# Kernel optimization log

Hardware: AMD Instinct MI355X
Metric: run time of the kernel (lower is better)

## Reference

```python
import jax, jax.numpy as jnp
import numpy as np

WIN = 8
SHIFT = 4
HEADS = 8


def _rel_pos_index(ws):
    # static numpy computation matching the torch buffer
    coords = np.stack(np.meshgrid(np.arange(ws), np.arange(ws), indexing='ij'))  # (2, ws, ws)
    cf = coords.reshape(2, -1)                      # (2, N)
    rel = cf[:, :, None] - cf[:, None, :]           # (2, N, N)
    rel = rel.transpose(1, 2, 0).copy()             # (N, N, 2)
    rel[:, :, 0] += ws - 1
    rel[:, :, 1] += ws - 1
    rel[:, :, 0] *= 2 * ws - 1
    return rel.sum(-1)                              # (N, N) int


def _attn_mask(H, W, ws, ss):
    # static shift mask, numpy (shapes are static under jit)
    img = np.zeros((H, W))
    cnt = 0
    sl = (slice(0, -ws), slice(-ws, -ss), slice(-ss, None))
    for h in sl:
        for w in sl:
            img[h, w] = cnt
            cnt += 1
    mw = img.reshape(H // ws, ws, W // ws, ws).transpose(0, 2, 1, 3).reshape(-1, ws * ws)
    diff = mw[:, None, :] - mw[:, :, None]          # (nW, N, N), matches unsqueeze(1)-unsqueeze(2)
    return np.where(diff != 0, -100.0, 0.0).astype(np.float32)


def setup_inputs() -> dict:
    key = jax.random.key(0)
    ks = jax.random.split(key, 6)
    B, C, H, W = 4, 192, 256, 256
    return {
        'x': jax.random.normal(ks[0], (B, C, H, W), jnp.float32),
        'qkv_w': jax.random.normal(ks[1], (3 * C, C), jnp.float32) * 0.02,
        'qkv_b': jnp.zeros((3 * C,), jnp.float32),
        'proj_w': jax.random.normal(ks[2], (C, C), jnp.float32) * 0.02,
        'proj_b': jnp.zeros((C,), jnp.float32),
        'rpb_table': jax.random.normal(ks[3], ((2 * WIN - 1) ** 2, HEADS), jnp.float32) * 0.02,
    }


def reference(x, qkv_w, qkv_b, proj_w, proj_b, rpb_table):
    B, C, H, W = x.shape
    ws, ss, h = WIN, SHIFT, HEADS
    N = ws * ws
    hd = C // h
    scale = hd ** -0.5

    xh = jnp.transpose(x, (0, 2, 3, 1))                       # (B,H,W,C)
    xs = jnp.roll(xh, shift=(-ss, -ss), axis=(1, 2))          # cyclic shift
    # window partition -> (B*nW, N, C)
    xw = xs.reshape(B, H // ws, ws, W // ws, ws, C).transpose(0, 1, 3, 2, 4, 5).reshape(-1, N, C)

    qkv = xw @ qkv_w.T + qkv_b                                # (B_, N, 3C)
    qkv = qkv.reshape(-1, N, 3, h, hd).transpose(2, 0, 3, 1, 4)
    q, k, v = qkv[0], qkv[1], qkv[2]                          # (B_, h, N, hd)

    attn = (q * scale) @ jnp.swapaxes(k, -2, -1)              # (B_, h, N, N)

    rpi = _rel_pos_index(ws)
    bias = rpb_table[rpi.reshape(-1)].reshape(N, N, h).transpose(2, 0, 1)  # (h, N, N)
    attn = attn + bias[None]

    mask = jnp.asarray(_attn_mask(H, W, ws, ss))              # (nW, N, N)
    nW = mask.shape[0]
    attn = attn.reshape(B, nW, h, N, N) + mask[None, :, None]
    attn = jax.nn.softmax(attn.reshape(-1, h, N, N), axis=-1)

    out = (attn @ v).transpose(0, 2, 1, 3).reshape(-1, N, C)  # (B_, N, C)
    out = out @ proj_w.T + proj_b

    # window reverse
    out = out.reshape(B, H // ws, W // ws, ws, ws, C).transpose(0, 1, 3, 2, 4, 5).reshape(B, H, W, C)
    out = jnp.roll(out, shift=(ss, ss), axis=(1, 2))          # reverse shift
    return x + jnp.transpose(out, (0, 3, 1, 2))               # residual, (B,C,H,W)
```

## Files before the change

kernel.cpp:

```cpp
#include <hip/hip_runtime.h>


typedef short short8 __attribute__((ext_vector_type(8)));
typedef float f32x4 __attribute__((ext_vector_type(4)));
typedef unsigned short us4 __attribute__((ext_vector_type(4)));

#define XB_OFF   0
#define KQ_OFF   12288
#define VT_OFF   24576
#define PB_OFF   24576
#define RPB_OFF  38400
#define QB_OFF   40200
#define LDS_BYTES 81552

#define WBF_BYTES 294912u
#define Y_FLOATS_PER_WIN 12288
#define Y_BYTES (4096ull * 49152ull)
#define WS_NEED (WBF_BYTES + Y_BYTES)

__device__ __forceinline__ unsigned short f2bfu(float f) {
  union { float f; unsigned u; } v; v.f = f;
  unsigned u = v.u;
  u += 0x7fffu + ((u >> 16) & 1u);
  return (unsigned short)(u >> 16);
}
__device__ __forceinline__ float bfu2f(unsigned short s) {
  union { unsigned u; float f; } v; v.u = ((unsigned)s) << 16;
  return v.f;
}

__device__ __forceinline__ int swzX(int t, int c) {
  return (((t >> 4) * 6 + (c >> 5)) << 9) | (((c >> 3) & 3) << 7) |
         ((t & 15) << 3) | (c & 7);
}
__device__ __forceinline__ int swzH(int i, int h, int g, int n, int j) {
  return (((i * 8 + h) * 3 + g) << 7) | (n << 3) | j;
}

__global__ void prep_weights(const float* __restrict__ qkv_w,
                             const float* __restrict__ proj_w,
                             unsigned short* __restrict__ wbf) {
  int d = blockIdx.x * 512 + threadIdx.x;
  int j    = d & 7;
  int lane = (d >> 3) & 63;
  int kk   = (d >> 9) % 6;
  int tile = d / 3072;
  int n16 = lane & 15, q4 = lane >> 4;
  int col = kk * 32 + q4 * 8 + j;
  float v = (tile < 36) ? qkv_w[(tile * 16 + n16) * 192 + col]
                        : proj_w[((tile - 36) * 16 + n16) * 192 + col];
  wbf[d] = f2bfu(v);
}

template <bool TOY>
__global__ __launch_bounds__(512)
__attribute__((amdgpu_waves_per_eu(4, 4)))
void winattn_kernel(
    const float* __restrict__ x, const float* __restrict__ qkv_b,
    const float* __restrict__ proj_b, const float* __restrict__ rpb,
    const unsigned short* __restrict__ wbf, float* __restrict__ dst)
{
  extern __shared__ __align__(16) char smem[];
  unsigned short* lds = (unsigned short*)smem;

  const int tid  = threadIdx.x;
  const int lane = tid & 63;
  const int wave = tid >> 6;
  const int n16  = lane & 15;
  const int q4   = lane >> 4;

  const int blk = blockIdx.x;
  const int L   = (blk & 7) * 512 + (blk >> 3);
  const int b    = L >> 10;
  const int wIdx = L & 1023;
  const int wr   = wIdx >> 5;
  const int wc   = wIdx & 31;

  {
    const int trow = wave;
    const int c3 = lane >> 3, w3 = lane & 7;
    const int hh  = (wr * 8 + 4 + trow) & 255;
    const int ww  = (wc * 8 + 4 + w3) & 255;
    const int t   = trow * 8 + w3;
    #pragma unroll
    for (int it = 0; it < 12; it++) {
      const int c = it * 16 + c3 * 2;
      const float* xp = x + (((size_t)(b * 192 + c)) << 16) + (hh << 8) + ww;
      float v0 = xp[0];
      float v1 = xp[65536];
      unsigned pk = (unsigned)f2bfu(v0) | ((unsigned)f2bfu(v1) << 16);
      *(unsigned*)(lds + XB_OFF + swzX(t, c)) = pk;
    }
    for (int i = tid; i < 1800; i += 512)
      lds[RPB_OFF + (i & 7) * 225 + (i >> 3)] = f2bfu(rpb[i]);
    for (int i = tid; i < 576; i += 512)
      lds[QB_OFF + i] = f2bfu(qkv_b[i]);
  }
  __syncthreads();

  {
    #pragma unroll 1
    for (int ot = wave; ot < 24; ot += 8) {
      f32x4 acc[4] = {{0,0,0,0},{0,0,0,0},{0,0,0,0},{0,0,0,0}};
      #pragma unroll
      for (int kk = 0; kk < 6; kk++) {
        short8 af = *(const short8*)(wbf + ((ot + 12) * 6 + kk) * 512 + lane * 8);
        #pragma unroll
        for (int tt = 0; tt < 4; tt++) {
          short8 bxk = *(const short8*)(lds + XB_OFF + ((tt * 6 + kk) * 64 + lane) * 8);
          acc[tt] = __builtin_amdgcn_mfma_f32_16x16x32_bf16(af, bxk, acc[tt], 0, 0, 0);
        }
      }
      const int ob = (ot + 12) * 16 + q4 * 4;
      const float b0 = bfu2f(lds[QB_OFF + ob + 0]);
      const float b1 = bfu2f(lds[QB_OFF + ob + 1]);
      const float b2 = bfu2f(lds[QB_OFF + ob + 2]);
      const float b3 = bfu2f(lds[QB_OFF + ob + 3]);
      if (ot < 12) {
        const int kc = ot * 16 + q4 * 4;
        const int hk = kc / 24, g = (kc >> 3) % 3, j0 = kc & 7;
        #pragma unroll
        for (int tt = 0; tt < 4; tt++) {
          us4 hv = { f2bfu(acc[tt][0] + b0), f2bfu(acc[tt][1] + b1),
                     f2bfu(acc[tt][2] + b2), f2bfu(acc[tt][3] + b3) };
          *(us4*)(lds + KQ_OFF + swzH(tt, hk, g, n16, j0)) = hv;
        }
      } else {
        const int vc = (ot - 12) * 16 + q4 * 4;
        #pragma unroll
        for (int tt = 0; tt < 4; tt++) {
          const int t = tt * 16 + n16;
          lds[VT_OFF + (vc + 0) * 72 + t] = f2bfu(acc[tt][0] + b0);
          lds[VT_OFF + (vc + 1) * 72 + t] = f2bfu(acc[tt][1] + b1);
          lds[VT_OFF + (vc + 2) * 72 + t] = f2bfu(acc[tt][2] + b2);
          lds[VT_OFF + (vc + 3) * 72 + t] = f2bfu(acc[tt][3] + b3);
        }
      }
    }
  }
  __syncthreads();

  const int h = wave;
  const short8 zero8 = {0,0,0,0,0,0,0,0};
  short8 kb[4], vb[2][2];
  {
    #pragma unroll
    for (int i = 0; i < 4; i++)
      kb[i] = (q4 < 3) ? *(const short8*)(lds + KQ_OFF + swzH(i, h, q4, n16, 0))
                       : zero8;
    #pragma unroll
    for (int nc = 0; nc < 2; nc++)
      #pragma unroll
      for (int kk = 0; kk < 2; kk++)
        vb[nc][kk] = (nc * 16 + n16 < 24)
          ? *(const short8*)(lds + VT_OFF + (h * 24 + nc * 16 + n16) * 72 + kk * 32 + q4 * 8)
          : zero8;
  }
  __syncthreads();

  {
    #pragma unroll 1
    for (int ot = wave; ot < 12; ot += 8) {
      f32x4 acc[4] = {{0,0,0,0},{0,0,0,0},{0,0,0,0},{0,0,0,0}};
      #pragma unroll
      for (int kk = 0; kk < 6; kk++) {
        short8 af = *(const short8*)(wbf + (ot * 6 + kk) * 512 + lane * 8);
        #pragma unroll
        for (int tt = 0; tt < 4; tt++) {
          short8 bxk = *(const short8*)(lds + XB_OFF + ((tt * 6 + kk) * 64 + lane) * 8);
          acc[tt] = __builtin_amdgcn_mfma_f32_16x16x32_bf16(af, bxk, acc[tt], 0, 0, 0);
        }
      }
      const int ob = ot * 16 + q4 * 4;
      const float b0 = bfu2f(lds[QB_OFF + ob + 0]);
      const float b1 = bfu2f(lds[QB_OFF + ob + 1]);
      const float b2 = bfu2f(lds[QB_OFF + ob + 2]);
      const float b3 = bfu2f(lds[QB_OFF + ob + 3]);
      const int qc = ot * 16 + q4 * 4;
      const int hq = qc / 24, g = (qc >> 3) % 3, j0 = qc & 7;
      #pragma unroll
      for (int tt = 0; tt < 4; tt++) {
        us4 hv = { f2bfu(acc[tt][0] + b0), f2bfu(acc[tt][1] + b1),
                   f2bfu(acc[tt][2] + b2), f2bfu(acc[tt][3] + b3) };
        *(us4*)(lds + KQ_OFF + swzH(tt, hq, g, n16, j0)) = hv;
      }
    }
  }
  __syncthreads();

  {
    short8 qa[4];
    #pragma unroll
    for (int i = 0; i < 4; i++)
      qa[i] = (q4 < 3) ? *(const short8*)(lds + KQ_OFF + swzH(i, h, q4, n16, 0))
                       : zero8;
    __syncthreads();

    const float scale = 0.20412414523193154f;
    unsigned short* Pw = lds + PB_OFF + wave * 1152;
    const unsigned short* rh = lds + RPB_OFF + h * 225;
    int cr[4], cc[4], clab[4];
    #pragma unroll
    for (int nj = 0; nj < 4; nj++) {
      int col = nj * 16 + n16;
      cr[nj] = col >> 3; cc[nj] = col & 7;
      int hs = wr * 8 + cr[nj], wsc = wc * 8 + cc[nj];
      int lh = (hs < 248) ? 0 : (hs < 252 ? 1 : 2);
      int lw = (wsc < 248) ? 0 : (wsc < 252 ? 1 : 2);
      clab[nj] = lh * 3 + lw;
    }
    #pragma unroll
    for (int mi = 0; mi < 4; mi++) {
      f32x4 smi[4];
      #pragma unroll
      for (int nj = 0; nj < 4; nj++) {
        f32x4 z = {0,0,0,0};
        smi[nj] = __builtin_amdgcn_mfma_f32_16x16x32_bf16(qa[mi], kb[nj], z, 0, 0, 0);
      }
      #pragma unroll
      for (int r = 0; r < 4; r++) {
        int row = mi * 16 + q4 * 4 + r;
        int r1 = row >> 3, c1 = row & 7;
        int hs = wr * 8 + r1, wsc = wc * 8 + c1;
        int lh = (hs < 248) ? 0 : (hs < 252 ? 1 : 2);
        int lw = (wsc < 248) ? 0 : (wsc < 252 ? 1 : 2);
        int rlab = lh * 3 + lw;
        float vals[4];
        float mx = -1e30f;
        #pragma unroll
        for (int nj = 0; nj < 4; nj++) {
          float v = smi[nj][r] * scale
                  + bfu2f(rh[(r1 - cr[nj] + 7) * 15 + (c1 - cc[nj] + 7)])
                  + ((rlab == clab[nj]) ? 0.0f : -100.0f);
          vals[nj] = v;
          mx = fmaxf(mx, v);
        }
        mx = fmaxf(mx, __shfl_xor(mx, 1));
        mx = fmaxf(mx, __shfl_xor(mx, 2));
        mx = fmaxf(mx, __shfl_xor(mx, 4));
        mx = fmaxf(mx, __shfl_xor(mx, 8));
        float sum = 0.f;
        #pragma unroll
        for (int nj = 0; nj < 4; nj++) { float p = __expf(vals[nj] - mx); vals[nj] = p; sum += p; }
        sum += __shfl_xor(sum, 1);
        sum += __shfl_xor(sum, 2);
        sum += __shfl_xor(sum, 4);
        sum += __shfl_xor(sum, 8);
        float inv = 1.0f / sum;
        #pragma unroll
        for (int nj = 0; nj < 4; nj++)
          Pw[(q4 * 4 + r) * 72 + nj * 16 + n16] = f2bfu(vals[nj] * inv);
      }
      short8 pa0 = *(const short8*)(Pw + n16 * 72 + q4 * 8);
      short8 pa1 = *(const short8*)(Pw + n16 * 72 + 32 + q4 * 8);
      #pragma unroll
      for (int nc = 0; nc < 2; nc++) {
        f32x4 a = {0,0,0,0};
        a = __builtin_amdgcn_mfma_f32_16x16x32_bf16(pa0, vb[nc][0], a, 0, 0, 0);
        a = __builtin_amdgcn_mfma_f32_16x16x32_bf16(pa1, vb[nc][1], a, 0, 0, 0);
        const int ch = nc * 16 + n16;
        if (ch < 24) {
          const int c = h * 24 + ch;
          #pragma unroll
          for (int r = 0; r < 4; r++) {
            const int t = mi * 16 + q4 * 4 + r;
            lds[KQ_OFF + swzX(t, c)] = f2bfu(a[r]);
          }
        }
      }
    }
  }
  __syncthreads();

  {
    #pragma unroll 1
    for (int ot = wave; ot < 12; ot += 8) {
      f32x4 acc[4] = {{0,0,0,0},{0,0,0,0},{0,0,0,0},{0,0,0,0}};
      #pragma unroll
      for (int kk = 0; kk < 6; kk++) {
        short8 af = *(const short8*)(wbf + ((36 + ot) * 6 + kk) * 512 + lane * 8);
        #pragma unroll
        for (int tt = 0; tt < 4; tt++) {
          short8 bok = *(const short8*)(lds + KQ_OFF + ((tt * 6 + kk) * 64 + lane) * 8);
          acc[tt] = __builtin_amdgcn_mfma_f32_16x16x32_bf16(af, bok, acc[tt], 0, 0, 0);
        }
      }
      if constexpr (TOY) {
        float* yw = dst + (size_t)L * Y_FLOATS_PER_WIN;
        #pragma unroll
        for (int r = 0; r < 4; r++) {
          const int o = ot * 16 + q4 * 4 + r;
          const float pb = proj_b[o];
          #pragma unroll
          for (int tt = 0; tt < 4; tt++) {
            const int t = tt * 16 + n16;
            yw[o * 64 + t] = bfu2f(lds[XB_OFF + swzX(t, o)]) + acc[tt][r] + pb;
          }
        }
      } else {
        #pragma unroll
        for (int r = 0; r < 4; r++) {
          const int o = ot * 16 + q4 * 4 + r;
          const float pb = proj_b[o];
          const size_t cbase = ((size_t)(b * 192 + o)) << 16;
          #pragma unroll
          for (int tt = 0; tt < 4; tt++) {
            const int t = tt * 16 + n16;
            const int hh = (wr * 8 + (t >> 3) + 4) & 255;
            const int ww = (wc * 8 + (t & 7) + 4) & 255;
            dst[cbase + (hh << 8) + ww] = bfu2f(lds[XB_OFF + swzX(t, o)]) + acc[tt][r] + pb;
          }
        }
      }
    }
  }
}

__global__ __launch_bounds__(512) void unshift_kernel(
    const float* __restrict__ Y, float* __restrict__ out)
{
  const int bid = blockIdx.x;
  const int cg = bid & 7;
  const int wr = (bid >> 3) & 31;
  const int b  = bid >> 8;
  const size_t winrow = ((size_t)(b * 32 + wr)) * 32;

  #pragma unroll
  for (int it = 0; it < 12; it++) {
    const int i = it * 512 + threadIdx.x;
    const int c_rel = i >> 8;
    const int rem   = i & 255;
    const int trow  = rem >> 5;
    const int k     = rem & 31;
    const int c     = cg * 24 + c_rel;
    const float* src = Y + (winrow + k) * Y_FLOATS_PER_WIN + c * 64 + trow * 8;
    f32x4 v0 = *(const f32x4*)(src);
    f32x4 v1 = *(const f32x4*)(src + 4);
    const int hh = (wr * 8 + trow + 4) & 255;
    float* drow = out + (((size_t)(b * 192 + c)) << 16) + (hh << 8);
    *(f32x4*)(drow + ((k * 8 + 4) & 255)) = v0;
    *(f32x4*)(drow + ((k * 8 + 8) & 255)) = v1;
  }
}

extern "C" void kernel_launch(void* const* d_in, const int* in_sizes, int n_in,
                              void* d_out, int out_size, void* d_ws, size_t ws_size,
                              hipStream_t stream) {
  const float* x      = (const float*)d_in[0];
  const float* qkv_w  = (const float*)d_in[1];
  const float* qkv_b  = (const float*)d_in[2];
  const float* proj_w = (const float*)d_in[3];
  const float* proj_b = (const float*)d_in[4];
  const float* rpb    = (const float*)d_in[5];
  float* out = (float*)d_out;
  unsigned short* wbf = (unsigned short*)d_ws;

  hipFuncSetAttribute(reinterpret_cast<const void*>(&winattn_kernel<true>),
                      hipFuncAttributeMaxDynamicSharedMemorySize, LDS_BYTES);
  hipFuncSetAttribute(reinterpret_cast<const void*>(&winattn_kernel<false>),
                      hipFuncAttributeMaxDynamicSharedMemorySize, LDS_BYTES);

  prep_weights<<<dim3(288), dim3(512), 0, stream>>>(qkv_w, proj_w, wbf);

  if (ws_size >= (size_t)WS_NEED) {
    float* Y = (float*)((char*)d_ws + WBF_BYTES);
    winattn_kernel<true><<<dim3(4096), dim3(512), LDS_BYTES, stream>>>(
        x, qkv_b, proj_b, rpb, wbf, Y);
    unshift_kernel<<<dim3(1024), dim3(512), 0, stream>>>(Y, out);
  } else {
    winattn_kernel<false><<<dim3(4096), dim3(512), LDS_BYTES, stream>>>(
        x, qkv_b, proj_b, rpb, wbf, out);
  }
}
```

Baseline: 597.0 us.

## Shrink LDS footprint by aliasing K/V/Q/P buffers and reading residual from global

```diff
diff --git a/kernel.cpp b/kernel.cpp
--- a/kernel.cpp
+++ b/kernel.cpp
@@ -7,11 +7,8 @@
 
 #define XB_OFF   0
 #define KQ_OFF   12288
-#define VT_OFF   24576
-#define PB_OFF   24576
-#define RPB_OFF  38400
-#define QB_OFF   40200
-#define LDS_BYTES 81552
+#define RPB_OFF  24576
+#define LDS_BYTES 52752
 
 #define WBF_BYTES 294912u
 #define Y_FLOATS_PER_WIN 12288
@@ -35,6 +32,9 @@
 }
 __device__ __forceinline__ int swzH(int i, int h, int g, int n, int j) {
   return (((i * 8 + h) * 3 + g) << 7) | (n << 3) | j;
+}
+__device__ __forceinline__ int swzV(int ch, int tok) {
+  return ch * 64 + (tok ^ ((ch & 7) << 3));
 }
 
 __global__ void prep_weights(const float* __restrict__ qkv_w,
@@ -54,7 +54,7 @@
 
 template <bool TOY>
 __global__ __launch_bounds__(512)
-__attribute__((amdgpu_waves_per_eu(4, 4)))
+__attribute__((amdgpu_waves_per_eu(6, 8)))
 void winattn_kernel(
     const float* __restrict__ x, const float* __restrict__ qkv_b,
     const float* __restrict__ proj_b, const float* __restrict__ rpb,
@@ -93,69 +93,43 @@
     }
     for (int i = tid; i < 1800; i += 512)
       lds[RPB_OFF + (i & 7) * 225 + (i >> 3)] = f2bfu(rpb[i]);
-    for (int i = tid; i < 576; i += 512)
-      lds[QB_OFF + i] = f2bfu(qkv_b[i]);
-  }
-  __syncthreads();
+  }
+  __syncthreads();
+
+  const int h = wave;
+  const short8 zero8 = {0,0,0,0,0,0,0,0};
+  short8 kb[4], vb[2][2], qa[4];
 
   {
     #pragma unroll 1
-    for (int ot = wave; ot < 24; ot += 8) {
+    for (int ot = wave; ot < 12; ot += 8) {
       f32x4 acc[4] = {{0,0,0,0},{0,0,0,0},{0,0,0,0},{0,0,0,0}};
       #pragma unroll
       for (int kk = 0; kk < 6; kk++) {
-        short8 af = *(const short8*)(wbf + ((ot + 12) * 6 + kk) * 512 + lane * 8);
+        short8 af = *(const short8*)(wbf + ((12 + ot) * 6 + kk) * 512 + lane * 8);
         #pragma unroll
         for (int tt = 0; tt < 4; tt++) {
           short8 bxk = *(const short8*)(lds + XB_OFF + ((tt * 6 + kk) * 64 + lane) * 8);
           acc[tt] = __builtin_amdgcn_mfma_f32_16x16x32_bf16(af, bxk, acc[tt], 0, 0, 0);
         }
       }
-      const int ob = (ot + 12) * 16 + q4 * 4;
-      const float b0 = bfu2f(lds[QB_OFF + ob + 0]);
-      const float b1 = bfu2f(lds[QB_OFF + ob + 1]);
-      const float b2 = bfu2f(lds[QB_OFF + ob + 2]);
-      const float b3 = bfu2f(lds[QB_OFF + ob + 3]);
-      if (ot < 12) {
-        const int kc = ot * 16 + q4 * 4;
-        const int hk = kc / 24, g = (kc >> 3) % 3, j0 = kc & 7;
-        #pragma unroll
-        for (int tt = 0; tt < 4; tt++) {
-          us4 hv = { f2bfu(acc[tt][0] + b0), f2bfu(acc[tt][1] + b1),
-                     f2bfu(acc[tt][2] + b2), f2bfu(acc[tt][3] + b3) };
-          *(us4*)(lds + KQ_OFF + swzH(tt, hk, g, n16, j0)) = hv;
-        }
-      } else {
-        const int vc = (ot - 12) * 16 + q4 * 4;
-        #pragma unroll
-        for (int tt = 0; tt < 4; tt++) {
-          const int t = tt * 16 + n16;
-          lds[VT_OFF + (vc + 0) * 72 + t] = f2bfu(acc[tt][0] + b0);
-          lds[VT_OFF + (vc + 1) * 72 + t] = f2bfu(acc[tt][1] + b1);
-          lds[VT_OFF + (vc + 2) * 72 + t] = f2bfu(acc[tt][2] + b2);
-          lds[VT_OFF + (vc + 3) * 72 + t] = f2bfu(acc[tt][3] + b3);
-        }
-      }
-    }
-  }
-  __syncthreads();
-
-  const int h = wave;
-  const short8 zero8 = {0,0,0,0,0,0,0,0};
-  short8 kb[4], vb[2][2];
-  {
-    #pragma unroll
-    for (int i = 0; i < 4; i++)
-      kb[i] = (q4 < 3) ? *(const short8*)(lds + KQ_OFF + swzH(i, h, q4, n16, 0))
-                       : zero8;
-    #pragma unroll
-    for (int nc = 0; nc < 2; nc++)
-      #pragma unroll
-      for (int kk = 0; kk < 2; kk++)
-        vb[nc][kk] = (nc * 16 + n16 < 24)
-          ? *(const short8*)(lds + VT_OFF + (h * 24 + nc * 16 + n16) * 72 + kk * 32 + q4 * 8)
-          : zero8;
-  }
+      const int kc = ot * 16 + q4 * 4;
+      const f32x4 bv = *(const f32x4*)(qkv_b + 192 + kc);
+      const int hk = kc / 24, g = (kc >> 3) % 3, j0 = kc & 7;
+      #pragma unroll
+      for (int tt = 0; tt < 4; tt++) {
+        us4 hv = { f2bfu(acc[tt][0] + bv[0]), f2bfu(acc[tt][1] + bv[1]),
+                   f2bfu(acc[tt][2] + bv[2]), f2bfu(acc[tt][3] + bv[3]) };
+        *(us4*)(lds + KQ_OFF + swzH(tt, hk, g, n16, j0)) = hv;
+      }
+    }
+  }
+  __syncthreads();
+
+  #pragma unroll
+  for (int i = 0; i < 4; i++)
+    kb[i] = (q4 < 3) ? *(const short8*)(lds + KQ_OFF + swzH(i, h, q4, n16, 0))
+                     : zero8;
   __syncthreads();
 
   {
@@ -164,40 +138,72 @@
       f32x4 acc[4] = {{0,0,0,0},{0,0,0,0},{0,0,0,0},{0,0,0,0}};
       #pragma unroll
       for (int kk = 0; kk < 6; kk++) {
-        short8 af = *(const short8*)(wbf + (ot * 6 + kk) * 512 + lane * 8);
+        short8 af = *(const short8*)(wbf + ((24 + ot) * 6 + kk) * 512 + lane * 8);
         #pragma unroll
         for (int tt = 0; tt < 4; tt++) {
           short8 bxk = *(const short8*)(lds + XB_OFF + ((tt * 6 + kk) * 64 + lane) * 8);
           acc[tt] = __builtin_amdgcn_mfma_f32_16x16x32_bf16(af, bxk, acc[tt], 0, 0, 0);
         }
       }
-      const int ob = ot * 16 + q4 * 4;
-      const float b0 = bfu2f(lds[QB_OFF + ob + 0]);
-      const float b1 = bfu2f(lds[QB_OFF + ob + 1]);
-      const float b2 = bfu2f(lds[QB_OFF + ob + 2]);
-      const float b3 = bfu2f(lds[QB_OFF + ob + 3]);
+      const int vc = ot * 16 + q4 * 4;
+      const f32x4 bv = *(const f32x4*)(qkv_b + 384 + vc);
+      #pragma unroll
+      for (int tt = 0; tt < 4; tt++) {
+        const int t = tt * 16 + n16;
+        #pragma unroll
+        for (int rr = 0; rr < 4; rr++)
+          lds[KQ_OFF + swzV(vc + rr, t)] = f2bfu(acc[tt][rr] + bv[rr]);
+      }
+    }
+  }
+  __syncthreads();
+
+  #pragma unroll
+  for (int nc = 0; nc < 2; nc++)
+    #pragma unroll
+    for (int kk = 0; kk < 2; kk++) {
+      const int ch = h * 24 + nc * 16 + n16;
+      vb[nc][kk] = (nc * 16 + n16 < 24)
+        ? *(const short8*)(lds + KQ_OFF + swzV(ch, kk * 32 + q4 * 8))
+        : zero8;
+    }
+  __syncthreads();
+
+  {
+    #pragma unroll 1
+    for (int ot = wave; ot < 12; ot += 8) {
+      f32x4 acc[4] = {{0,0,0,0},{0,0,0,0},{0,0,0,0},{0,0,0,0}};
+      #pragma unroll
+      for (int kk = 0; kk < 6; kk++) {
+        short8 af = *(const short8*)(wbf + (ot * 6 + kk) * 512 + lane * 8);
+        #pragma unroll
+        for (int tt = 0; tt < 4; tt++) {
+          short8 bxk = *(const short8*)(lds + XB_OFF + ((tt * 6 + kk) * 64 + lane) * 8);
+          acc[tt] = __builtin_amdgcn_mfma_f32_16x16x32_bf16(af, bxk, acc[tt], 0, 0, 0);
+        }
+      }
       const int qc = ot * 16 + q4 * 4;
+      const f32x4 bv = *(const f32x4*)(qkv_b + qc);
       const int hq = qc / 24, g = (qc >> 3) % 3, j0 = qc & 7;
       #pragma unroll
       for (int tt = 0; tt < 4; tt++) {
-        us4 hv = { f2bfu(acc[tt][0] + b0), f2bfu(acc[tt][1] + b1),
-                   f2bfu(acc[tt][2] + b2), f2bfu(acc[tt][3] + b3) };
+        us4 hv = { f2bfu(acc[tt][0] + bv[0]), f2bfu(acc[tt][1] + bv[1]),
+                   f2bfu(acc[tt][2] + bv[2]), f2bfu(acc[tt][3] + bv[3]) };
         *(us4*)(lds + KQ_OFF + swzH(tt, hq, g, n16, j0)) = hv;
       }
     }
   }
   __syncthreads();
 
-  {
-    short8 qa[4];
-    #pragma unroll
-    for (int i = 0; i < 4; i++)
-      qa[i] = (q4 < 3) ? *(const short8*)(lds + KQ_OFF + swzH(i, h, q4, n16, 0))
-                       : zero8;
-    __syncthreads();
-
+  #pragma unroll
+  for (int i = 0; i < 4; i++)
+    qa[i] = (q4 < 3) ? *(const short8*)(lds + KQ_OFF + swzH(i, h, q4, n16, 0))
+                     : zero8;
+  __syncthreads();
+
+  {
     const float scale = 0.20412414523193154f;
-    unsigned short* Pw = lds + PB_OFF + wave * 1152;
+    unsigned short* Pw = lds + KQ_OFF + wave * 1152;
     const unsigned short* rh = lds + RPB_OFF + h * 225;
     int cr[4], cc[4], clab[4];
     #pragma unroll
@@ -264,7 +270,7 @@
           #pragma unroll
           for (int r = 0; r < 4; r++) {
             const int t = mi * 16 + q4 * 4 + r;
-            lds[KQ_OFF + swzX(t, c)] = f2bfu(a[r]);
+            lds[XB_OFF + swzX(t, c)] = f2bfu(a[r]);
           }
         }
       }
@@ -281,7 +287,7 @@
         short8 af = *(const short8*)(wbf + ((36 + ot) * 6 + kk) * 512 + lane * 8);
         #pragma unroll
         for (int tt = 0; tt < 4; tt++) {
-          short8 bok = *(const short8*)(lds + KQ_OFF + ((tt * 6 + kk) * 64 + lane) * 8);
+          short8 bok = *(const short8*)(lds + XB_OFF + ((tt * 6 + kk) * 64 + lane) * 8);
           acc[tt] = __builtin_amdgcn_mfma_f32_16x16x32_bf16(af, bok, acc[tt], 0, 0, 0);
         }
       }
@@ -294,7 +300,7 @@
           #pragma unroll
           for (int tt = 0; tt < 4; tt++) {
             const int t = tt * 16 + n16;
-            yw[o * 64 + t] = bfu2f(lds[XB_OFF + swzX(t, o)]) + acc[tt][r] + pb;
+            yw[o * 64 + t] = acc[tt][r] + pb;
           }
         }
       } else {
@@ -308,7 +314,8 @@
             const int t = tt * 16 + n16;
             const int hh = (wr * 8 + (t >> 3) + 4) & 255;
             const int ww = (wc * 8 + (t & 7) + 4) & 255;
-            dst[cbase + (hh << 8) + ww] = bfu2f(lds[XB_OFF + swzX(t, o)]) + acc[tt][r] + pb;
+            const size_t idx = cbase + (hh << 8) + ww;
+            dst[idx] = x[idx] + acc[tt][r] + pb;
           }
         }
       }
@@ -317,7 +324,8 @@
 }
 
 __global__ __launch_bounds__(512) void unshift_kernel(
-    const float* __restrict__ Y, float* __restrict__ out)
+    const float* __restrict__ Y, const float* __restrict__ x,
+    float* __restrict__ out)
 {
   const int bid = blockIdx.x;
   const int cg = bid & 7;
@@ -337,9 +345,13 @@
     f32x4 v0 = *(const f32x4*)(src);
     f32x4 v1 = *(const f32x4*)(src + 4);
     const int hh = (wr * 8 + trow + 4) & 255;
-    float* drow = out + (((size_t)(b * 192 + c)) << 16) + (hh << 8);
-    *(f32x4*)(drow + ((k * 8 + 4) & 255)) = v0;
-    *(f32x4*)(drow + ((k * 8 + 8) & 255)) = v1;
+    const size_t rowbase = (((size_t)(b * 192 + c)) << 16) + (hh << 8);
+    const int o0 = (k * 8 + 4) & 255;
+    const int o1 = (k * 8 + 8) & 255;
+    f32x4 x0 = *(const f32x4*)(x + rowbase + o0);
+    f32x4 x1 = *(const f32x4*)(x + rowbase + o1);
+    *(f32x4*)(out + rowbase + o0) = x0 + v0;
+    *(f32x4*)(out + rowbase + o1) = x1 + v1;
   }
 }
 
@@ -366,7 +378,7 @@
     float* Y = (float*)((char*)d_ws + WBF_BYTES);
     winattn_kernel<true><<<dim3(4096), dim3(512), LDS_BYTES, stream>>>(
         x, qkv_b, proj_b, rpb, wbf, Y);
-    unshift_kernel<<<dim3(1024), dim3(512), 0, stream>>>(Y, out);
+    unshift_kernel<<<dim3(1024), dim3(512), 0, stream>>>(Y, x, out);
   } else {
     winattn_kernel<false><<<dim3(4096), dim3(512), LDS_BYTES, stream>>>(
         x, qkv_b, proj_b, rpb, wbf, out);
```

New measurement: 812.2 us. +36.1%, slower.
